# Performance work log

Hardware: AMD Instinct MI355X
Metric: run time of the kernel (lower is better)

Reference implementation:

```python
import jax, jax.numpy as jnp
import numpy as np

N = 100000   # nodes
E = 1600000  # edges
G = 512      # graphs
L = 3        # num_unit LEConv layers
D = 64       # hidden dim


def setup_inputs() -> dict:
    key = jax.random.key(0)
    ks = jax.random.split(key, 12)
    s = 1.0 / np.sqrt(D)
    x = jax.random.normal(ks[0], (N, 4), jnp.float32)
    edge_index = jax.random.randint(ks[1], (2, E), 0, N, dtype=jnp.int64)
    edge_attr = jax.random.uniform(ks[2], (E,), jnp.float32)
    batch = jnp.sort(jax.random.randint(ks[3], (N,), 0, G, dtype=jnp.int64))
    return {
        "x": x,
        "edge_index": edge_index,
        "edge_attr": edge_attr,
        "batch": batch,
        "W_emb": jax.random.normal(ks[4], (4, D), jnp.float32) * 0.5,
        "b_emb": jnp.zeros((D,), jnp.float32),
        "W1": jax.random.normal(ks[5], (L, D, D), jnp.float32) * s,  # LEConv lin1 (on x_j)
        "b1": jnp.zeros((L, D), jnp.float32),
        "W2": jax.random.normal(ks[6], (L, D, D), jnp.float32) * s,  # LEConv lin2 (on x_i, no bias)
        "W3": jax.random.normal(ks[7], (L, D, D), jnp.float32) * s,  # LEConv lin3 (root)
        "b3": jnp.zeros((L, D), jnp.float32),
        "Wl1": jax.random.normal(ks[8], (D, 32), jnp.float32) * s,
        "bl1": jnp.zeros((32,), jnp.float32),
        "Wl2": jax.random.normal(ks[9], (32, 3), jnp.float32) * (1.0 / np.sqrt(32)),
        "bl2": jnp.zeros((3,), jnp.float32),
    }


def reference(x, edge_index, edge_attr, batch, W_emb, b_emb,
              W1, b1, W2, W3, b3, Wl1, bl1, Wl2, bl2):
    src, dst = edge_index[0], edge_index[1]
    h = x @ W_emb + b_emb                          # [N, D]
    for l in range(L):
        a = h @ W1[l] + b1[l]                      # lin1(x) -> gathered at source j
        b = h @ W2[l]                              # lin2(x) -> gathered at target i
        # LEConv message: e_ij * (lin1(x_j) - lin2(x_i)), aggr='add' at target
        msg = edge_attr[:, None] * (a[src] - b[dst])   # [E, D]
        agg = jax.ops.segment_sum(msg, dst, num_segments=N)
        h = jax.nn.relu(agg + h @ W3[l] + b3[l])
    # global_mean_pool over graphs
    sums = jax.ops.segment_sum(h, batch, num_segments=G)              # [G, D]
    counts = jax.ops.segment_sum(jnp.ones((N,), h.dtype), batch, num_segments=G)
    graph_x = sums / jnp.maximum(counts, 1.0)[:, None]
    pred = jax.nn.relu(graph_x @ Wl1 + bl1) @ Wl2 + bl2               # [G, 3]
    return pred
```

## Files before the change

### kernel.cpp

```cpp
#include <hip/hip_runtime.h>
#include <hip/hip_bf16.h>

#define NNODES 100000
#define NEDGES 1600000
#define NGRAPH 512
#define DIM    64
#define NLAYER 3

#define NB   1000
#define BN   100
#define CAP  2048
#define SC_BLOCKS 256
#define EPB  6250
#define PACK_BLOCKS 18
#define ZERO_BLOCKS 2
#define NBLK32 3125
#define EMB_BLOCKS 6250

typedef __attribute__((ext_vector_type(8))) short short8;
typedef __attribute__((ext_vector_type(4))) float float4v;
typedef unsigned long long u64;

__device__ __forceinline__ __hip_bfloat16 f2b(float f) { return __float2bfloat16(f); }
__device__ __forceinline__ unsigned short f2b_bits(float f) {
    __hip_bfloat16 h = __float2bfloat16(f);
    return *reinterpret_cast<unsigned short*>(&h);
}

__device__ __forceinline__ unsigned pack_rec(int src, unsigned wbits32) {
    unsigned w15 = ((wbits32 + 0x8000u) >> 16) & 0x7FFFu;
    return ((unsigned)src << 15) | w15;
}

#define ACC4(ACC, RR, VV) do {                                              \
    float _w = __uint_as_float(((RR) & 0x7FFFu) << 16);                     \
    unsigned _lo = (unsigned)(VV), _hi = (unsigned)((VV) >> 32);            \
    ACC[0] = fmaf(_w, __uint_as_float(_lo << 16), ACC[0]);                  \
    ACC[1] = fmaf(_w, __uint_as_float(_lo & 0xFFFF0000u), ACC[1]);          \
    ACC[2] = fmaf(_w, __uint_as_float(_hi << 16), ACC[2]);                  \
    ACC[3] = fmaf(_w, __uint_as_float(_hi & 0xFFFF0000u), ACC[3]);          \
} while (0)

#define ROUND_L(rbase, i0, cnt, aA, aB, aC, aD) do {                        \
    int _iA = (i0) + q, _iB = (i0) + 4 + q;                                 \
    int _iC = (i0) + 8 + q, _iD = (i0) + 12 + q;                            \
    unsigned _rA = 0u, _rB = 0u, _rC = 0u, _rD = 0u;                        \
    if (_iA < (cnt)) _rA = (rbase)[_iA];                                    \
    if (_iB < (cnt)) _rB = (rbase)[_iB];                                    \
    if (_iC < (cnt)) _rC = (rbase)[_iC];                                    \
    if (_iD < (cnt)) _rD = (rbase)[_iD];                                    \
    u64 _vA = 0, _vB = 0, _vC = 0, _vD = 0;                                 \
    if (_iA < (cnt)) _vA = h64[(size_t)(_rA >> 15) * 16 + p];               \
    if (_iB < (cnt)) _vB = h64[(size_t)(_rB >> 15) * 16 + p];               \
    if (_iC < (cnt)) _vC = h64[(size_t)(_rC >> 15) * 16 + p];               \
    if (_iD < (cnt)) _vD = h64[(size_t)(_rD >> 15) * 16 + p];               \
    ACC4(aA, _rA, _vA); ACC4(aB, _rB, _vB);                                 \
    ACC4(aC, _rC, _vC); ACC4(aD, _rD, _vD);                                 \
} while (0)

#define ROUND_G(i0, en, aA, aB, aC, aD) do {                                \
    int _iA = (i0) + q, _iB = (i0) + 4 + q;                                 \
    int _iC = (i0) + 8 + q, _iD = (i0) + 12 + q;                            \
    unsigned _rA = 0u, _rB = 0u, _rC = 0u, _rD = 0u;                        \
    if (_iA < (en)) _rA = perm2[_iA];                                       \
    if (_iB < (en)) _rB = perm2[_iB];                                       \
    if (_iC < (en)) _rC = perm2[_iC];                                       \
    if (_iD < (en)) _rD = perm2[_iD];                                       \
    u64 _vA = 0, _vB = 0, _vC = 0, _vD = 0;                                 \
    if (_iA < (en)) _vA = h64[(size_t)(_rA >> 15) * 16 + p];                \
    if (_iB < (en)) _vB = h64[(size_t)(_rB >> 15) * 16 + p];                \
    if (_iC < (en)) _vC = h64[(size_t)(_rC >> 15) * 16 + p];                \
    if (_iD < (en)) _vD = h64[(size_t)(_rD >> 15) * 16 + p];                \
    ACC4(aA, _rA, _vA); ACC4(aB, _rB, _vB);                                 \
    ACC4(aC, _rC, _vC); ACC4(aD, _rD, _vD);                                 \
} while (0)

#define REDUCE_STORE(a0, a1, a2, a3, rowidx) do {                           \
    float _r0 = (a0[0] + a1[0]) + (a2[0] + a3[0]);                          \
    float _r1 = (a0[1] + a1[1]) + (a2[1] + a3[1]);                          \
    float _r2 = (a0[2] + a1[2]) + (a2[2] + a3[2]);                          \
    float _r3 = (a0[3] + a1[3]) + (a2[3] + a3[3]);                          \
    _r0 += __shfl_xor(_r0, 16, 64); _r1 += __shfl_xor(_r1, 16, 64);         \
    _r2 += __shfl_xor(_r2, 16, 64); _r3 += __shfl_xor(_r3, 16, 64);         \
    _r0 += __shfl_xor(_r0, 32, 64); _r1 += __shfl_xor(_r1, 32, 64);         \
    _r2 += __shfl_xor(_r2, 32, 64); _r3 += __shfl_xor(_r3, 32, 64);         \
    if (q == 0) {                                                           \
        u64 _w = (u64)f2b_bits(_r0) | ((u64)f2b_bits(_r1) << 16) |          \
                 ((u64)f2b_bits(_r2) << 32) | ((u64)f2b_bits(_r3) << 48);   \
        int _off = ((rowidx) * 128 + p * 8) ^ (((rowidx) & 7) << 4);        \
        *(u64*)(mbytes + _off) = _w;                                        \
    }                                                                       \
} while (0)


__global__ __launch_bounds__(256) void local_sort_kernel(
    const int* __restrict__ ei, const float* __restrict__ ea,
    int2* __restrict__ perm_raw, int2* __restrict__ offcnt,
    const float* __restrict__ W1, const float* __restrict__ W2,
    const float* __restrict__ W3, __hip_bfloat16* __restrict__ wpack,
    float* __restrict__ gsum) {
    int tid = threadIdx.x, k = blockIdx.x;
    if (k >= SC_BLOCKS + PACK_BLOCKS) {
        float4v z = {0.f, 0.f, 0.f, 0.f};
        int idx = (k - SC_BLOCKS - PACK_BLOCKS) * 256 + tid;
        for (int i = idx; i < NGRAPH * DIM / 4; i += ZERO_BLOCKS * 256)
            ((float4v*)gsum)[i] = z;
        return;
    }
    if (k >= SC_BLOCKS) {
        int unit = (k - SC_BLOCKS) * 4 + (tid >> 6);
        if (unit < NLAYER * 24) {
            int kh = unit & 1, tn = (unit >> 1) & 3, w = (unit >> 3) % 3, l = unit / 24;
            const float* Wsrc = (w == 0 ? W1 : (w == 1 ? W2 : W3)) + l * 4096;
            int L = tid & 63;
            __hip_bfloat16* dst = wpack + (size_t)unit * 512 + L * 8;
            int kb = 32 * kh + (L >> 4) * 8;
            int nb = 16 * tn + (L & 15);
            #pragma unroll
            for (int j = 0; j < 8; ++j)
                dst[j] = f2b(Wsrc[(kb + j) * 64 + nb]);
        }
        return;
    }
    __shared__ int cnt[NB];
    __shared__ int off[NB];
    __shared__ int partial[256];
    __shared__ int2 srec[EPB];
    int e0 = k * EPB;
    for (int i = tid; i < NB; i += 256) cnt[i] = 0;
    __syncthreads();
    for (int i = tid; i < EPB; i += 256)
        atomicAdd(&cnt[ei[NEDGES + e0 + i] / BN], 1);
    __syncthreads();
    int loc[4]; int s = 0;
    #pragma unroll
    for (int j = 0; j < 4; ++j) {
        int b = tid * 4 + j;
        int v = (b < NB) ? cnt[b] : 0;
        loc[j] = s; s += v;
    }
    partial[tid] = s;
    __syncthreads();
    for (int o = 1; o < 256; o <<= 1) {
        int t = (tid >= o) ? partial[tid - o] : 0;
        __syncthreads();
        partial[tid] += t;
        __syncthreads();
    }
    int excl = partial[tid] - s;
    #pragma unroll
    for (int j = 0; j < 4; ++j) {
        int b = tid * 4 + j;
        if (b < NB) off[b] = excl + loc[j];
    }
    __syncthreads();
    for (int b = tid; b < NB; b += 256)
        offcnt[(size_t)k * NB + b] = make_int2(off[b], cnt[b]);
    __syncthreads();
    for (int i = tid; i < EPB; i += 256) {
        int e = e0 + i;
        int src = ei[e];
        int d = ei[NEDGES + e];
        float w = ea[e];
        int bin = d / BN;
        int dloc = d - bin * BN;
        int pos = atomicAdd(&off[bin], 1);
        srec[pos] = make_int2(src | (dloc << 20), __float_as_int(w));
    }
    __syncthreads();
    for (int i = tid; i < EPB; i += 256)
        perm_raw[e0 + i] = srec[i];
}

__global__ __launch_bounds__(256) void csr_embed_kernel(
    const int2* __restrict__ perm_raw, const int2* __restrict__ offcnt,
    unsigned* __restrict__ perm2, int2* __restrict__ rows, float* __restrict__ wdeg,
    const float* __restrict__ x, const float* __restrict__ Wemb,
    const float* __restrict__ bemb, __hip_bfloat16* __restrict__ h) {
    __shared__ int2     recs[CAP];
    __shared__ unsigned recs2u[CAP];
    __shared__ int   pscan[256];
    __shared__ int   sprefix[SC_BLOCKS + 1];
    __shared__ int   boff[SC_BLOCKS];
    __shared__ int   cnt[BN];
    __shared__ int   start[BN];
    __shared__ int   cur[BN];
    __shared__ float ws[BN];
    int b = blockIdx.x, tid = threadIdx.x;
    if (b >= NB) {
        int t = (b - NB) * 256 + tid;
        int node = t >> 4, d0 = (t & 15) * 4;
        float4v xv = *(const float4v*)&x[(size_t)node * 4];
        u64 w0 = 0;
        #pragma unroll
        for (int j = 0; j < 4; ++j) {
            int ch = d0 + j;
            float s = bemb[ch];
            #pragma unroll
            for (int k = 0; k < 4; ++k) s = fmaf(xv[k], Wemb[k * 64 + ch], s);
            w0 |= (u64)f2b_bits(s) << (16 * j);
        }
        ((u64*)h)[(size_t)node * 16 + (t & 15)] = w0;
        return;
    }
    if (tid < BN) { cnt[tid] = 0; ws[tid] = 0.f; }
    int2 oc = offcnt[(size_t)tid * NB + b];
    boff[tid] = oc.x;
    int c = oc.y;
    pscan[tid] = c;
    __syncthreads();
    for (int o = 1; o < 256; o <<= 1) {
        int t = (tid >= o) ? pscan[tid - o] : 0;
        __syncthreads();
        pscan[tid] += t;
        __syncthreads();
    }
    sprefix[tid] = pscan[tid] - c;
    if (tid == 255) sprefix[256] = pscan[255];
    __syncthreads();
    int n = min(sprefix[SC_BLOCKS], CAP);
    for (int i = tid; i < n; i += 256) {
        int lo = 0, hi = SC_BLOCKS;
        while (hi - lo > 1) { int m = (lo + hi) >> 1; if (sprefix[m] <= i) lo = m; else hi = m; }
        int2 rec = perm_raw[lo * EPB + boff[lo] + (i - sprefix[lo])];
        recs[i] = rec;
        atomicAdd(&cnt[rec.x >> 20], 1);
        atomicAdd(&ws[rec.x >> 20], __int_as_float(rec.y));
    }
    __syncthreads();
    {
        int v = (tid < BN) ? cnt[tid] : 0;
        pscan[tid] = v;
        __syncthreads();
        for (int o = 1; o < 128; o <<= 1) {
            int t = (tid >= o) ? pscan[tid - o] : 0;
            __syncthreads();
            pscan[tid] += t;
            __syncthreads();
        }
        if (tid < BN) start[tid] = pscan[tid] - v;
    }
    __syncthreads();
    if (tid < BN) {
        cur[tid] = start[tid];
        int base = b * CAP + start[tid];
        rows[b * BN + tid] = make_int2(base, base + cnt[tid]);
        wdeg[b * BN + tid] = ws[tid];
    }
    __syncthreads();
    for (int i = tid; i < n; i += 256) {
        int2 rec = recs[i];
        int pos = atomicAdd(&cur[rec.x >> 20], 1);
        recs2u[pos] = pack_rec(rec.x & 0xFFFFF, (unsigned)rec.y);
    }
    __syncthreads();
    for (int i = tid; i < n; i += 256)
        perm2[(size_t)b * CAP + i] = recs2u[i];
}


template <int LAST>
__global__ __launch_bounds__(256, 6) void layer_kernel(
    const __hip_bfloat16* __restrict__ hin, __hip_bfloat16* __restrict__ hout,
    const int2* __restrict__ rows, const unsigned* __restrict__ perm2,
    const float* __restrict__ wdeg, const __hip_bfloat16* __restrict__ wpack,
    const float* __restrict__ b1, const float* __restrict__ b3,
    const int* __restrict__ batch, float* __restrict__ gsum) {
    __shared__ __align__(16) unsigned char mbytes[32 * 128];
    __shared__ unsigned srecs[32][64];
    int tid = threadIdx.x;
    int lane = tid & 63, wv = tid >> 6;
    int q = lane >> 4, p = lane & 15;
    int n0 = blockIdx.x * 32 + wv * 8;
    const u64* h64 = (const u64*)hin;

    #pragma unroll
    for (int nl = 0; nl < 8; ++nl) {
        int2 rl = rows[n0 + nl];
        int cnt = min(rl.y - rl.x, 64);
        if (lane < cnt) srecs[wv * 8 + nl][lane] = perm2[rl.x + lane];
    }

    #pragma unroll
    for (int np = 0; np < 4; ++np) {
        int2 rlA = rows[n0 + np];
        int2 rlB = rows[n0 + np + 4];
        int cntA = min(rlA.y - rlA.x, 64);
        int cntB = min(rlB.y - rlB.x, 64);
        const unsigned* rbA = srecs[wv * 8 + np];
        const unsigned* rbB = srecs[wv * 8 + np + 4];
        float aA0[4] = {}, aA1[4] = {}, aA2[4] = {}, aA3[4] = {};
        float aB0[4] = {}, aB1[4] = {}, aB2[4] = {}, aB3[4] = {};
        #pragma unroll
        for (int rr = 0; rr < 4; ++rr) {
            int i0 = rr * 16;
            if (i0 < cntA) ROUND_L(rbA, i0, cntA, aA0, aA1, aA2, aA3);
            if (i0 < cntB) ROUND_L(rbB, i0, cntB, aB0, aB1, aB2, aB3);
        }
        for (int i0 = rlA.x + 64; i0 < rlA.y; i0 += 16)
            ROUND_G(i0, rlA.y, aA0, aA1, aA2, aA3);
        for (int i0 = rlB.x + 64; i0 < rlB.y; i0 += 16)
            ROUND_G(i0, rlB.y, aB0, aB1, aB2, aB3);
        REDUCE_STORE(aA0, aA1, aA2, aA3, wv * 8 + np);
        REDUCE_STORE(aB0, aB1, aB2, aB3, wv * 8 + np + 4);
    }
    __syncthreads();

    int tile = wv >> 1, ch = wv & 1;
    float4v acc[3][2] = {};
    const short8* wp = (const short8*)wpack;
    int row = tile * 16 + p;
    int node_c = blockIdx.x * 32 + row;
    #pragma unroll
    for (int kh = 0; kh < 2; ++kh) {
        int roff = (row * 128 + kh * 64 + q * 16) ^ ((row & 7) << 4);
        short8 am = *(const short8*)(mbytes + roff);
        short8 ah = *(const short8*)((const short*)hin + (size_t)node_c * 64 + kh * 32 + q * 8);
        #pragma unroll
        for (int w = 0; w < 3; ++w) {
            #pragma unroll
            for (int t = 0; t < 2; ++t) {
                int tn = ch * 2 + t;
                short8 bfrag = wp[(size_t)((w * 4 + tn) * 2 + kh) * 64 + lane];
                acc[w][t] = __builtin_amdgcn_mfma_f32_16x16x32_bf16(
                    w == 0 ? am : ah, bfrag, acc[w][t], 0, 0, 0);
            }
        }
    }

    float b1v[2], b3v[2];
    #pragma unroll
    for (int t = 0; t < 2; ++t) {
        int tn = ch * 2 + t;
        b1v[t] = b1[tn * 16 + p];
        b3v[t] = b3[tn * 16 + p];
    }
    int tb = blockIdx.x * 32 + tile * 16;
    if (!LAST) {
        unsigned short* hout_u = (unsigned short*)hout;
        #pragma unroll
        for (int reg = 0; reg < 4; ++reg) {
            int node = tb + q * 4 + reg;
            float wd = wdeg[node];
            #pragma unroll
            for (int t = 0; t < 2; ++t) {
                int tn = ch * 2 + t;
                float s = acc[0][t][reg] + acc[2][t][reg] + b3v[t] +
                          wd * (b1v[t] - acc[1][t][reg]);
                __builtin_nontemporal_store(f2b_bits(fmaxf(s, 0.f)),
                                            &hout_u[(size_t)node * 64 + tn * 16 + p]);
            }
        }
    } else {
        float val[4][2];
        int gb[4];
        #pragma unroll
        for (int reg = 0; reg < 4; ++reg) {
            int node = tb + q * 4 + reg;
            float wd = wdeg[node];
            gb[reg] = batch[node];
            #pragma unroll
            for (int t = 0; t < 2; ++t) {
                float s = acc[0][t][reg] + acc[2][t][reg] + b3v[t] +
                          wd * (b1v[t] - acc[1][t][reg]);
                val[reg][t] = fmaxf(s, 0.f);
            }
        }
        int glo = batch[tb];
        int ghi = batch[tb + 15];
        for (int g = glo; g <= ghi; ++g) {
            #pragma unroll
            for (int t = 0; t < 2; ++t) {
                int tn = ch * 2 + t;
                float part = 0.f;
                #pragma unroll
                for (int reg = 0; reg < 4; ++reg)
                    part += (gb[reg] == g) ? val[reg][t] : 0.f;
                part += __shfl_xor(part, 16, 64);
                part += __shfl_xor(part, 32, 64);
                if (q == 0) atomicAdd(&gsum[g * 64 + tn * 16 + p], part);
            }
        }
    }
}


__global__ __launch_bounds__(64) void mlp_kernel(
    const float* __restrict__ gsum, const int* __restrict__ batch,
    const float* __restrict__ Wl1, const float* __restrict__ bl1,
    const float* __restrict__ Wl2, const float* __restrict__ bl2,
    float* __restrict__ out) {
    __shared__ int lohi[2];
    __shared__ float gxl[64];
    __shared__ float hid[32];
    int g = blockIdx.x, t = threadIdx.x;
    if (t < 2) {
        int target = g + t;
        int lo = 0, hi = NNODES;
        while (lo < hi) { int m = (lo + hi) >> 1; if (batch[m] < target) lo = m + 1; else hi = m; }
        lohi[t] = lo;
    }
    __syncthreads();
    int cnt = lohi[1] - lohi[0];
    gxl[t] = gsum[g * 64 + t] / (float)max(cnt, 1);
    __syncthreads();
    if (t < 32) {
        float s = bl1[t];
        for (int k = 0; k < 64; ++k) s = fmaf(gxl[k], Wl1[k * 32 + t], s);
        hid[t] = fmaxf(s, 0.f);
    }
    __syncthreads();
    if (t < 3) {
        float s = bl2[t];
        for (int k = 0; k < 32; ++k) s = fmaf(hid[k], Wl2[k * 3 + t], s);
        out[g * 3 + t] = s;
    }
}


extern "C" void kernel_launch(void* const* d_in, const int* in_sizes, int n_in,
                              void* d_out, int out_size, void* d_ws, size_t ws_size,
                              hipStream_t stream) {
    const float* x    = (const float*)d_in[0];
    const int*   ei   = (const int*)d_in[1];
    const float* ea   = (const float*)d_in[2];
    const int*   bat  = (const int*)d_in[3];
    const float* Wemb = (const float*)d_in[4];
    const float* bemb = (const float*)d_in[5];
    const float* W1   = (const float*)d_in[6];
    const float* b1   = (const float*)d_in[7];
    const float* W2   = (const float*)d_in[8];
    const float* W3   = (const float*)d_in[9];
    const float* b3   = (const float*)d_in[10];
    const float* Wl1  = (const float*)d_in[11];
    const float* bl1  = (const float*)d_in[12];
    const float* Wl2  = (const float*)d_in[13];
    const float* bl2  = (const float*)d_in[14];
    float* out = (float*)d_out;

    char* ws = (char*)d_ws;
    __hip_bfloat16*  h_b      = (__hip_bfloat16*) (ws + 0);
    __hip_bfloat16*  h_a      = (__hip_bfloat16*) (ws + 12800000);
    int2*            perm_raw = (int2*)           (ws + 25600000);
    unsigned*        perm2    = (unsigned*)       (ws + 38400000);
    int2*            rows     = (int2*)           (ws + 46592000);
    int2*            offcnt   = (int2*)           (ws + 47392000);
    float*           wdeg     = (float*)          (ws + 49440000);
    __hip_bfloat16*  wpack    = (__hip_bfloat16*) (ws + 49840000);
    float*           gsum     = (float*)          (ws + 49913728);

    local_sort_kernel<<<SC_BLOCKS + PACK_BLOCKS + ZERO_BLOCKS, 256, 0, stream>>>(
        ei, ea, perm_raw, offcnt, W1, W2, W3, wpack, gsum);
    csr_embed_kernel<<<NB + EMB_BLOCKS, 256, 0, stream>>>(
        perm_raw, offcnt, perm2, rows, wdeg, x, Wemb, bemb, h_a);

    layer_kernel<0><<<NBLK32, 256, 0, stream>>>(
        h_a, h_b, rows, perm2, wdeg, wpack, b1, b3, bat, gsum);
    layer_kernel<0><<<NBLK32, 256, 0, stream>>>(
        h_b, h_a, rows, perm2, wdeg, wpack + (size_t)24 * 512, b1 + 64, b3 + 64, bat, gsum);
    layer_kernel<1><<<NBLK32, 256, 0, stream>>>(
        h_a, h_b, rows, perm2, wdeg, wpack + (size_t)48 * 512, b1 + 128, b3 + 128, bat, gsum);

    mlp_kernel<<<NGRAPH, 64, 0, stream>>>(gsum, bat, Wl1, bl1, Wl2, bl2, out);
}
```

Measured before the change: 296.2 us.

## Stage neighbor records in registers via shuffles and prefetch next node

The edge-gather loop no longer stages each node's packed edge records in shared memory. Each lane now holds one record in a register, records are broadcast with wave shuffles, and the next node's records are prefetched while the current node is processed. Nodes are handled one at a time instead of two interleaved, the per-element bounds checks are dropped (padding records are assumed to hold zero weight), and the odd-channel bf16 unpack skips the mask. Together with raising the launch-bounds occupancy hint from 6 to 8, this is meant to cut LDS traffic and register pressure. The cost is less memory-level parallelism per wave and reliance on zero-padded record slots.

```diff
diff --git a/kernel.cpp b/kernel.cpp
--- a/kernel.cpp
+++ b/kernel.cpp
@@ -32,30 +32,26 @@
     return ((unsigned)src << 15) | w15;
 }
 
-#define ACC4(ACC, RR, VV) do {                                              \
+#define ACC4D(ACC, RR, VV) do {                                             \
     float _w = __uint_as_float(((RR) & 0x7FFFu) << 16);                     \
     unsigned _lo = (unsigned)(VV), _hi = (unsigned)((VV) >> 32);            \
     ACC[0] = fmaf(_w, __uint_as_float(_lo << 16), ACC[0]);                  \
-    ACC[1] = fmaf(_w, __uint_as_float(_lo & 0xFFFF0000u), ACC[1]);          \
+    ACC[1] = fmaf(_w, __uint_as_float(_lo), ACC[1]);                        \
     ACC[2] = fmaf(_w, __uint_as_float(_hi << 16), ACC[2]);                  \
-    ACC[3] = fmaf(_w, __uint_as_float(_hi & 0xFFFF0000u), ACC[3]);          \
+    ACC[3] = fmaf(_w, __uint_as_float(_hi), ACC[3]);                        \
 } while (0)
 
-#define ROUND_L(rbase, i0, cnt, aA, aB, aC, aD) do {                        \
-    int _iA = (i0) + q, _iB = (i0) + 4 + q;                                 \
-    int _iC = (i0) + 8 + q, _iD = (i0) + 12 + q;                            \
-    unsigned _rA = 0u, _rB = 0u, _rC = 0u, _rD = 0u;                        \
-    if (_iA < (cnt)) _rA = (rbase)[_iA];                                    \
-    if (_iB < (cnt)) _rB = (rbase)[_iB];                                    \
-    if (_iC < (cnt)) _rC = (rbase)[_iC];                                    \
-    if (_iD < (cnt)) _rD = (rbase)[_iD];                                    \
-    u64 _vA = 0, _vB = 0, _vC = 0, _vD = 0;                                 \
-    if (_iA < (cnt)) _vA = h64[(size_t)(_rA >> 15) * 16 + p];               \
-    if (_iB < (cnt)) _vB = h64[(size_t)(_rB >> 15) * 16 + p];               \
-    if (_iC < (cnt)) _vC = h64[(size_t)(_rC >> 15) * 16 + p];               \
-    if (_iD < (cnt)) _vD = h64[(size_t)(_rD >> 15) * 16 + p];               \
-    ACC4(aA, _rA, _vA); ACC4(aB, _rB, _vB);                                 \
-    ACC4(aC, _rC, _vC); ACC4(aD, _rD, _vD);                                 \
+#define ROUND_S(REC, BASE, aA, aB, aC, aD) do {                             \
+    unsigned _rA = (unsigned)__shfl((int)(REC), (BASE) + q, 64);            \
+    unsigned _rB = (unsigned)__shfl((int)(REC), (BASE) + 4 + q, 64);        \
+    unsigned _rC = (unsigned)__shfl((int)(REC), (BASE) + 8 + q, 64);        \
+    unsigned _rD = (unsigned)__shfl((int)(REC), (BASE) + 12 + q, 64);       \
+    u64 _vA = h64[(size_t)(_rA >> 15) * 16 + p];                            \
+    u64 _vB = h64[(size_t)(_rB >> 15) * 16 + p];                            \
+    u64 _vC = h64[(size_t)(_rC >> 15) * 16 + p];                            \
+    u64 _vD = h64[(size_t)(_rD >> 15) * 16 + p];                            \
+    ACC4D(aA, _rA, _vA); ACC4D(aB, _rB, _vB);                               \
+    ACC4D(aC, _rC, _vC); ACC4D(aD, _rD, _vD);                               \
 } while (0)
 
 #define ROUND_G(i0, en, aA, aB, aC, aD) do {                                \
@@ -66,13 +62,12 @@
     if (_iB < (en)) _rB = perm2[_iB];                                       \
     if (_iC < (en)) _rC = perm2[_iC];                                       \
     if (_iD < (en)) _rD = perm2[_iD];                                       \
-    u64 _vA = 0, _vB = 0, _vC = 0, _vD = 0;                                 \
-    if (_iA < (en)) _vA = h64[(size_t)(_rA >> 15) * 16 + p];                \
-    if (_iB < (en)) _vB = h64[(size_t)(_rB >> 15) * 16 + p];                \
-    if (_iC < (en)) _vC = h64[(size_t)(_rC >> 15) * 16 + p];                \
-    if (_iD < (en)) _vD = h64[(size_t)(_rD >> 15) * 16 + p];                \
-    ACC4(aA, _rA, _vA); ACC4(aB, _rB, _vB);                                 \
-    ACC4(aC, _rC, _vC); ACC4(aD, _rD, _vD);                                 \
+    u64 _vA = h64[(size_t)(_rA >> 15) * 16 + p];                            \
+    u64 _vB = h64[(size_t)(_rB >> 15) * 16 + p];                            \
+    u64 _vC = h64[(size_t)(_rC >> 15) * 16 + p];                            \
+    u64 _vD = h64[(size_t)(_rD >> 15) * 16 + p];                            \
+    ACC4D(aA, _rA, _vA); ACC4D(aB, _rB, _vB);                               \
+    ACC4D(aC, _rC, _vC); ACC4D(aD, _rD, _vD);                               \
 } while (0)
 
 #define REDUCE_STORE(a0, a1, a2, a3, rowidx) do {                           \
@@ -260,49 +255,39 @@
 
 
 template <int LAST>
-__global__ __launch_bounds__(256, 6) void layer_kernel(
+__global__ __launch_bounds__(256, 8) void layer_kernel(
     const __hip_bfloat16* __restrict__ hin, __hip_bfloat16* __restrict__ hout,
     const int2* __restrict__ rows, const unsigned* __restrict__ perm2,
     const float* __restrict__ wdeg, const __hip_bfloat16* __restrict__ wpack,
     const float* __restrict__ b1, const float* __restrict__ b3,
     const int* __restrict__ batch, float* __restrict__ gsum) {
     __shared__ __align__(16) unsigned char mbytes[32 * 128];
-    __shared__ unsigned srecs[32][64];
     int tid = threadIdx.x;
     int lane = tid & 63, wv = tid >> 6;
     int q = lane >> 4, p = lane & 15;
     int n0 = blockIdx.x * 32 + wv * 8;
     const u64* h64 = (const u64*)hin;
 
-    #pragma unroll
+    int2 rl = rows[n0 + (lane & 7)];
+    int st_n = __shfl(rl.x, 0, 64);
+    int en_n = __shfl(rl.y, 0, 64);
+    unsigned rec_n = (lane < min(en_n - st_n, 32)) ? perm2[st_n + lane] : 0u;
+
     for (int nl = 0; nl < 8; ++nl) {
-        int2 rl = rows[n0 + nl];
-        int cnt = min(rl.y - rl.x, 64);
-        if (lane < cnt) srecs[wv * 8 + nl][lane] = perm2[rl.x + lane];
-    }
-
-    #pragma unroll
-    for (int np = 0; np < 4; ++np) {
-        int2 rlA = rows[n0 + np];
-        int2 rlB = rows[n0 + np + 4];
-        int cntA = min(rlA.y - rlA.x, 64);
-        int cntB = min(rlB.y - rlB.x, 64);
-        const unsigned* rbA = srecs[wv * 8 + np];
-        const unsigned* rbB = srecs[wv * 8 + np + 4];
-        float aA0[4] = {}, aA1[4] = {}, aA2[4] = {}, aA3[4] = {};
-        float aB0[4] = {}, aB1[4] = {}, aB2[4] = {}, aB3[4] = {};
-        #pragma unroll
-        for (int rr = 0; rr < 4; ++rr) {
-            int i0 = rr * 16;
-            if (i0 < cntA) ROUND_L(rbA, i0, cntA, aA0, aA1, aA2, aA3);
-            if (i0 < cntB) ROUND_L(rbB, i0, cntB, aB0, aB1, aB2, aB3);
-        }
-        for (int i0 = rlA.x + 64; i0 < rlA.y; i0 += 16)
-            ROUND_G(i0, rlA.y, aA0, aA1, aA2, aA3);
-        for (int i0 = rlB.x + 64; i0 < rlB.y; i0 += 16)
-            ROUND_G(i0, rlB.y, aB0, aB1, aB2, aB3);
-        REDUCE_STORE(aA0, aA1, aA2, aA3, wv * 8 + np);
-        REDUCE_STORE(aB0, aB1, aB2, aB3, wv * 8 + np + 4);
+        int st = st_n, en = en_n;
+        unsigned rec = rec_n;
+        if (nl < 7) {
+            st_n = __shfl(rl.x, nl + 1, 64);
+            en_n = __shfl(rl.y, nl + 1, 64);
+            rec_n = (lane < min(en_n - st_n, 32)) ? perm2[st_n + lane] : 0u;
+        }
+        int cnt = en - st;
+        float a0[4] = {}, a1[4] = {}, a2[4] = {}, a3[4] = {};
+        ROUND_S(rec, 0, a0, a1, a2, a3);
+        if (cnt > 16) ROUND_S(rec, 16, a0, a1, a2, a3);
+        for (int i0 = st + 32; i0 < en; i0 += 16)
+            ROUND_G(i0, en, a0, a1, a2, a3);
+        REDUCE_STORE(a0, a1, a2, a3, wv * 8 + nl);
     }
     __syncthreads();
 
```

New measurement: 246.8 us. 16.7% less time.
